# Kernel tuning notes

Measured on AMD Instinct MI355X. Metric: run time of the kernel, lower is better.

The kernel has to match this reference:

```python
import jax, jax.numpy as jnp
import numpy as np

N, E, B = 20000, 100000, 16
U_SZ, U_RED = 4096, 256
EDGE_H, EDGE_OUT = 1024, 512
NODE_H = 512
X_DIM, EA_DIM = 9, 1


def _lin(key, fan_out, fan_in):
    kw, kb = jax.random.split(key)
    s = 1.0 / np.sqrt(fan_in)
    w = jax.random.uniform(kw, (fan_out, fan_in), jnp.float32, -s, s)
    b = jax.random.uniform(kb, (fan_out,), jnp.float32, -s, s)
    return w, b


def setup_inputs() -> dict:
    key = jax.random.key(0)
    ks = jax.random.split(key, 16)
    inp = {}
    inp["x"] = jax.random.normal(ks[0], (N, X_DIM), jnp.float32)
    inp["edge_index"] = jax.random.randint(ks[1], (2, E), 0, N, jnp.int64)
    inp["edge_attr"] = jax.random.normal(ks[2], (E, EA_DIM), jnp.float32)
    inp["u"] = jax.random.normal(ks[3], (B, U_SZ), jnp.float32)
    inp["batch"] = jnp.sort(jax.random.randint(ks[4], (N,), 0, B, jnp.int64))
    # select_dim_reduction: Linear(4096, 256)
    inp["w_sel"], inp["b_sel"] = _lin(ks[5], U_RED, U_SZ)
    # edge MLP: 275 -> 1024 -> 1024 -> 1024 -> 1024 -> 512
    e_in = EA_DIM + 2 * X_DIM + U_RED  # 275
    inp["ew0"], inp["eb0"] = _lin(ks[6], EDGE_H, e_in)
    inp["ew1"], inp["eb1"] = _lin(ks[7], EDGE_H, EDGE_H)
    inp["ew2"], inp["eb2"] = _lin(ks[8], EDGE_H, EDGE_H)
    inp["ew3"], inp["eb3"] = _lin(ks[9], EDGE_H, EDGE_H)
    inp["ew4"], inp["eb4"] = _lin(ks[10], EDGE_OUT, EDGE_H)
    # node_mlp_1: (9+512) -> 512 -> 512 (relu after each)
    inp["nw0"], inp["nb0"] = _lin(ks[11], NODE_H, X_DIM + EDGE_OUT)
    inp["nw1"], inp["nb1"] = _lin(ks[12], NODE_H, NODE_H)
    # node_mlp_2: (9+512+256) -> 512 -> 1
    inp["mw0"], inp["mb0"] = _lin(ks[13], NODE_H, X_DIM + NODE_H + U_RED)
    inp["mw1"], inp["mb1"] = _lin(ks[14], 1, NODE_H)
    return inp


def reference(x, edge_index, edge_attr, u, batch,
              w_sel, b_sel,
              ew0, eb0, ew1, eb1, ew2, eb2, ew3, eb3, ew4, eb4,
              nw0, nb0, nw1, nb1, mw0, mb0, mw1, mb1):
    row, col = edge_index[0], edge_index[1]
    u_r = u @ w_sel.T + b_sel                       # [B, 256]
    eb_idx = batch[row]                             # edge -> graph
    # EdgeModel: cat([src, dest, edge_attr, u[batch]]) -> MLP
    e_in = jnp.concatenate([x[row], x[col], edge_attr, u_r[eb_idx]], axis=1)  # [E,275]
    h = jax.nn.relu(e_in @ ew0.T + eb0)
    h = jax.nn.relu(h @ ew1.T + eb1)
    h = jax.nn.relu(h @ ew2.T + eb2)
    h = jax.nn.relu(h @ ew3.T + eb3)
    edge_out = h @ ew4.T + eb4                      # [E, 512]
    # NodeModel: gather x[col], edge MLP, scatter_mean onto row
    n_in = jnp.concatenate([x[col], edge_out], axis=1)  # [E, 521]
    h = jax.nn.relu(n_in @ nw0.T + nb0)
    h = jax.nn.relu(h @ nw1.T + nb1)                # [E, 512]
    seg_sum = jax.ops.segment_sum(h, row, num_segments=x.shape[0])
    cnt = jax.ops.segment_sum(jnp.ones((h.shape[0],), h.dtype), row, num_segments=x.shape[0])
    agg = seg_sum / jnp.maximum(cnt, 1.0)[:, None]  # scatter_mean
    m_in = jnp.concatenate([x, agg, u_r[batch]], axis=1)  # [N, 777]
    h2 = jax.nn.relu(m_in @ mw0.T + mb0)
    out = h2 @ mw1.T + mb1                          # [N, 1]
    return jnp.squeeze(out)
```

## Files before the change

### kernel.cpp

```cpp
#include <hip/hip_runtime.h>


#define NN 20000
#define EE 100000
#define BB 16

typedef _Float16 f16x8 __attribute__((ext_vector_type(8)));
typedef _Float16 f16x4 __attribute__((ext_vector_type(4)));
typedef float f32x4 __attribute__((ext_vector_type(4)));

__device__ __forceinline__ int clampi(int v, int hi) {
    return v < 0 ? 0 : (v >= hi ? hi - 1 : v);
}

__device__ __forceinline__ void gld_lds16(const void* g, void* l) {
    __builtin_amdgcn_global_load_lds(
        (const __attribute__((address_space(1))) unsigned int*)g,
        (__attribute__((address_space(3))) unsigned int*)l, 16, 0, 0);
}

__global__ __launch_bounds__(256, 2) void gemm256n(
    const _Float16* __restrict__ Ag, const _Float16* __restrict__ Wt,
    int KT, int KTs, const float* __restrict__ bias,
    _Float16* __restrict__ C, int KTo, int ktOff)
{
    __shared__ _Float16 As[16384];
    __shared__ _Float16 Bs[8192];

    const int tid  = threadIdx.x;
    const int lane = tid & 63;
    const int wid  = tid >> 6;
    const int wm   = wid & 1;
    const int wn   = wid >> 1;
    const int l15  = lane & 15;
    const int l4   = (lane >> 4) << 2;

    const int nb  = gridDim.x;
    const int MT2 = gridDim.y;
    int f = blockIdx.y * nb + blockIdx.x;
    const int MT8 = MT2 & ~7;
    int p, c;
    if (f < MT8 * nb) {
        c = (f >> 3) % nb;
        p = (f & 7) + 8 * ((f >> 3) / nb);
    } else {
        int g = f - MT8 * nb;
        p = MT8 + g / nb;
        c = g % nb;
    }

    f32x4 acc[8][4];
#pragma unroll
    for (int i = 0; i < 8; ++i)
#pragma unroll
        for (int j = 0; j < 4; ++j) acc[i][j] = (f32x4){0.f, 0.f, 0.f, 0.f};

    const int kg = (lane >> 4) << 10;

    auto stage = [&](int kt) {
        const int par = (kt & 1);
        const _Float16* a0 = Ag + ((size_t)(2 * p)     * KTs + kt) * 4096 + tid * 8;
        const _Float16* a1 = Ag + ((size_t)(2 * p + 1) * KTs + kt) * 4096 + tid * 8;
        const _Float16* b0 = Wt + ((size_t)c * KT + kt) * 4096 + tid * 8;
        _Float16* dA = As + par * 8192 + wid * 512;
        _Float16* dB = Bs + par * 4096 + wid * 512;
        gld_lds16(a0,        dA);
        gld_lds16(a0 + 2048, dA + 2048);
        gld_lds16(a1,        dA + 4096);
        gld_lds16(a1 + 2048, dA + 6144);
        gld_lds16(b0,        dB);
        gld_lds16(b0 + 2048, dB + 2048);
    };

    stage(0);
    for (int kt = 0; kt < KT; ++kt) {
        if (kt + 1 < KT) {
            stage(kt + 1);
            asm volatile("s_waitcnt vmcnt(6)" ::: "memory");
        } else {
            asm volatile("s_waitcnt vmcnt(0)" ::: "memory");
        }
        __builtin_amdgcn_s_barrier();
        const int par = (kt & 1);
        const _Float16* Ap = As + par * 8192 + wm * 4096 + kg + l15 * 8;
        const _Float16* Bp = Bs + par * 4096 + kg + (wn * 64 + l15) * 8;
        f16x8 af[4], bf[4];
#pragma unroll
        for (int j = 0; j < 4; ++j) bf[j] = *(const f16x8*)(Bp + j * 128);
#pragma unroll
        for (int i = 0; i < 4; ++i) af[i] = *(const f16x8*)(Ap + i * 128);
        __builtin_amdgcn_s_setprio(1);
#pragma unroll
        for (int i = 0; i < 4; ++i)
#pragma unroll
            for (int j = 0; j < 4; ++j)
                acc[i][j] = __builtin_amdgcn_mfma_f32_16x16x32_f16(
                    af[i], bf[j], acc[i][j], 0, 0, 0);
        __builtin_amdgcn_s_setprio(0);
#pragma unroll
        for (int i = 0; i < 4; ++i) af[i] = *(const f16x8*)(Ap + (4 + i) * 128);
        __builtin_amdgcn_s_setprio(1);
#pragma unroll
        for (int i = 0; i < 4; ++i)
#pragma unroll
            for (int j = 0; j < 4; ++j)
                acc[4 + i][j] = __builtin_amdgcn_mfma_f32_16x16x32_f16(
                    af[i], bf[j], acc[4 + i][j], 0, 0, 0);
        __builtin_amdgcn_s_setprio(0);
        __builtin_amdgcn_s_barrier();
    }

    _Float16* tr = As;
#pragma unroll
    for (int pass = 0; pass < 4; ++pass) {
        __syncthreads();
        if (wm == (pass >> 1)) {
            const int fi = (pass & 1) << 2;
#pragma unroll
            for (int i = 0; i < 4; ++i) {
#pragma unroll
                for (int v = 0; v < 4; ++v) {
                    const int lr = i * 16 + l4 + v;
#pragma unroll
                    for (int j = 0; j < 4; ++j) {
                        const int cc = wn * 64 + j * 16 + l15;
                        float val = acc[fi + i][j][v] + bias[c * 128 + cc];
                        val = fmaxf(val, 0.f);
                        tr[lr * 132 + cc] = (_Float16)val;
                    }
                }
            }
        }
        __syncthreads();
#pragma unroll
        for (int it = 0; it < 4; ++it) {
            const int id = it * 256 + tid;
            const int r  = id & 63;
            const int cg = id >> 6;
            f16x4 lo = *(const f16x4*)(tr + r * 132 + cg * 8);
            f16x4 hi = *(const f16x4*)(tr + r * 132 + cg * 8 + 4);
            f16x8 v8;
#pragma unroll
            for (int t = 0; t < 4; ++t) { v8[t] = lo[t]; v8[t + 4] = hi[t]; }
            const int kti = ktOff + c * 4 + (cg >> 2);
            const int mt_out = 2 * p + (pass >> 1);
            const int r128 = ((pass & 1) << 6) + r;
            *(f16x8*)(C + (((size_t)mt_out * KTo + kti) * 4 + (cg & 3)) * 1024
                        + (size_t)r128 * 8) = v8;
        }
    }
}

template <int MODE>
__global__ __launch_bounds__(256, 4) void gemm_blk(
    const _Float16* __restrict__ A,
    const _Float16* __restrict__ Wt,
    int KT, int KTs,
    const float* __restrict__ bias, int ldbias, const int* __restrict__ gbid,
    void* __restrict__ C, int KTo, int ktOff,
    int ldc,
    const int* __restrict__ srow, float* __restrict__ aux,
    int M, int relu)
{
    __shared__ char smem[32768];
    _Float16* As = (_Float16*)smem;
    _Float16* Bs = As + 8192;

    const int tid  = threadIdx.x;
    const int lane = tid & 63;
    const int wid  = tid >> 6;
    const int wm = (wid & 1) << 6;
    const int wn = (wid >> 1) << 6;

    const int nb = gridDim.x;
    const int MT = gridDim.y;
    int f = blockIdx.y * nb + blockIdx.x;
    const int MT8 = MT & ~7;
    int p, c;
    if (f < MT8 * nb) {
        c = (f >> 3) % nb;
        p = (f & 7) + 8 * ((f >> 3) / nb);
    } else {
        int g = f - MT8 * nb;
        p = MT8 + g / nb;
        c = g % nb;
    }

    f32x4 acc[4][4];
#pragma unroll
    for (int i = 0; i < 4; ++i)
#pragma unroll
        for (int j = 0; j < 4; ++j) acc[i][j] = (f32x4){0.f, 0.f, 0.f, 0.f};

    const _Float16* pA = A + (size_t)p * KTs * 4096;
    const _Float16* pB = Wt + (size_t)c * KT * 4096;
    const int cb0 = wid * 64;
    const int cb1 = 256 + wid * 64;
    const int kq  = (lane >> 4) * 128;
    const int l15 = lane & 15;
    const int l4  = (lane >> 4) << 2;

    int kt = 0;
    for (; kt + 2 <= KT; kt += 2) {
        __syncthreads();
        gld_lds16(pA + (size_t)(cb0 + lane) * 8,        As + cb0 * 8);
        gld_lds16(pA + (size_t)(cb1 + lane) * 8,        As + cb1 * 8);
        gld_lds16(pA + 4096 + (size_t)(cb0 + lane) * 8, As + 4096 + cb0 * 8);
        gld_lds16(pA + 4096 + (size_t)(cb1 + lane) * 8, As + 4096 + cb1 * 8);
        gld_lds16(pB + (size_t)(cb0 + lane) * 8,        Bs + cb0 * 8);
        gld_lds16(pB + (size_t)(cb1 + lane) * 8,        Bs + cb1 * 8);
        gld_lds16(pB + 4096 + (size_t)(cb0 + lane) * 8, Bs + 4096 + cb0 * 8);
        gld_lds16(pB + 4096 + (size_t)(cb1 + lane) * 8, Bs + 4096 + cb1 * 8);
        pA += 8192; pB += 8192;
        __syncthreads();

#pragma unroll
        for (int s = 0; s < 2; ++s) {
            f16x8 af[4], bf[4];
            const int sb = s * 4096;
#pragma unroll
            for (int i = 0; i < 4; ++i)
                af[i] = *(const f16x8*)(As + sb + (size_t)((kq + wm + i * 16 + l15) << 3));
#pragma unroll
            for (int j = 0; j < 4; ++j)
                bf[j] = *(const f16x8*)(Bs + sb + (size_t)((kq + wn + j * 16 + l15) << 3));
#pragma unroll
            for (int i = 0; i < 4; ++i)
#pragma unroll
                for (int j = 0; j < 4; ++j)
                    acc[i][j] = __builtin_amdgcn_mfma_f32_16x16x32_f16(af[i], bf[j], acc[i][j], 0, 0, 0);
        }
    }
    if (kt < KT) {
        __syncthreads();
        gld_lds16(pA + (size_t)(cb0 + lane) * 8, As + cb0 * 8);
        gld_lds16(pA + (size_t)(cb1 + lane) * 8, As + cb1 * 8);
        gld_lds16(pB + (size_t)(cb0 + lane) * 8, Bs + cb0 * 8);
        gld_lds16(pB + (size_t)(cb1 + lane) * 8, Bs + cb1 * 8);
        __syncthreads();
        f16x8 af[4], bf[4];
#pragma unroll
        for (int i = 0; i < 4; ++i)
            af[i] = *(const f16x8*)(As + (size_t)((kq + wm + i * 16 + l15) << 3));
#pragma unroll
        for (int j = 0; j < 4; ++j)
            bf[j] = *(const f16x8*)(Bs + (size_t)((kq + wn + j * 16 + l15) << 3));
#pragma unroll
        for (int i = 0; i < 4; ++i)
#pragma unroll
            for (int j = 0; j < 4; ++j)
                acc[i][j] = __builtin_amdgcn_mfma_f32_16x16x32_f16(af[i], bf[j], acc[i][j], 0, 0, 0);
    }

    if (MODE == 0) {
        _Float16* tr = (_Float16*)smem;
#pragma unroll
        for (int pass = 0; pass < 2; ++pass) {
            __syncthreads();
            if (wm == pass * 64) {
#pragma unroll
                for (int i = 0; i < 4; ++i) {
#pragma unroll
                    for (int v = 0; v < 4; ++v) {
                        const int lr = i * 16 + l4 + v;
                        const float* brow = bias;
                        if (gbid) {
                            int m = p * 128 + pass * 64 + lr;
                            if (m >= M) m = M - 1;
                            brow = bias + (size_t)clampi(gbid[m], BB) * ldbias;
                        }
#pragma unroll
                        for (int j = 0; j < 4; ++j) {
                            const int cc = wn + j * 16 + l15;
                            float val = acc[i][j][v] + brow[c * 128 + cc];
                            if (relu) val = fmaxf(val, 0.f);
                            tr[lr * 132 + cc] = (_Float16)val;
                        }
                    }
                }
            }
            __syncthreads();
#pragma unroll
            for (int it = 0; it < 4; ++it) {
                const int id = it * 256 + tid;
                const int r  = id & 63;
                const int cg = id >> 6;
                f16x4 lo = *(const f16x4*)(tr + r * 132 + cg * 8);
                f16x4 hi = *(const f16x4*)(tr + r * 132 + cg * 8 + 4);
                f16x8 v8;
#pragma unroll
                for (int t = 0; t < 4; ++t) { v8[t] = lo[t]; v8[t + 4] = hi[t]; }
                const int kti = ktOff + (c << 2) + (cg >> 2);
                const int gr  = pass * 64 + r;
                size_t o = (((size_t)p * KTo + kti) * 4 + (cg & 3)) * 1024 + (size_t)gr * 8;
                *(f16x8*)((_Float16*)C + o) = v8;
            }
        }
    } else if (MODE == 1) {
#pragma unroll
        for (int i = 0; i < 4; ++i) {
#pragma unroll
            for (int v = 0; v < 4; ++v) {
                const int m = p * 128 + wm + i * 16 + l4 + v;
                if (m >= M) continue;
                const float* brow = bias;
                if (gbid) brow = bias + (size_t)clampi(gbid[m], BB) * ldbias;
#pragma unroll
                for (int j = 0; j < 4; ++j) {
                    const int col = c * 128 + wn + j * 16 + l15;
                    float val = acc[i][j][v] + brow[col];
                    if (relu) val = fmaxf(val, 0.f);
                    ((float*)C)[(size_t)m * ldc + col] = val;
                }
            }
        }
    } else if (MODE == 2) {
        float* trf = (float*)smem;
#pragma unroll
        for (int pass = 0; pass < 4; ++pass) {
            __syncthreads();
            if (wm == ((pass >> 1) << 6)) {
                const int i0 = (pass & 1) << 1;
#pragma unroll
                for (int ii = 0; ii < 2; ++ii) {
                    const int i = i0 + ii;
                    const int lr = ii * 16 + l4;
#pragma unroll
                    for (int v = 0; v < 4; ++v) {
#pragma unroll
                        for (int j = 0; j < 4; ++j) {
                            const int cc = wn + j * 16 + l15;
                            float val = acc[i][j][v] + bias[c * 128 + cc];
                            if (relu) val = fmaxf(val, 0.f);
                            trf[(lr + v) * 130 + cc] = val;
                        }
                    }
                }
            }
            __syncthreads();
            const int ebase = p * 128 + pass * 32;
#pragma unroll
            for (int it = 0; it < 16; ++it) {
                const int id = it * 256 + tid;
                const int lr = id >> 7;
                const int colg = id & 127;
                const int el = ebase + lr;
                if (el < M) {
                    const int node = clampi(srow[el], NN);
                    atomicAdd(&aux[(size_t)node * 512 + c * 128 + colg],
                              trf[lr * 130 + colg]);
                }
            }
        }
    } else {
        const float* mw1 = aux;
        float* out = (float*)C;
#pragma unroll
        for (int i = 0; i < 4; ++i) {
#pragma unroll
            for (int v = 0; v < 4; ++v) {
                const int m = p * 128 + wm + i * 16 + l4 + v;
                const int mc = m < M ? m : M - 1;
                const float* brow = bias + (size_t)clampi(gbid[mc], BB) * ldbias;
                float s = 0.f;
#pragma unroll
                for (int j = 0; j < 4; ++j) {
                    const int col = c * 128 + wn + j * 16 + l15;
                    float val = acc[i][j][v] + brow[col];
                    val = fmaxf(val, 0.f);
                    s += val * mw1[col];
                }
                s += __shfl_down(s, 8, 16);
                s += __shfl_down(s, 4, 16);
                s += __shfl_down(s, 2, 16);
                s += __shfl_down(s, 1, 16);
                if (l15 == 0 && m < M) atomicAdd(&out[m], s);
            }
        }
    }
}


__global__ void k_w2h_blk(const float* __restrict__ src, _Float16* __restrict__ dst,
                          int N, int Ksrc, int Kd, int mode)
{
    int t = blockIdx.x * blockDim.x + threadIdx.x;
    if (t >= N * Kd) return;
    int n = t / Kd, k = t - n * Kd;
    float v = 0.f;
    if (mode == 0)      { if (k < Ksrc) v = src[(size_t)n * Ksrc + k]; }
    else if (mode == 1) { if (k < 19) v = src[(size_t)n * 275 + k]; }
    else if (mode == 2) { if (k < 9) v = src[(size_t)n * Ksrc + k];
                          else if (k >= 32 && k < 544) v = src[(size_t)n * Ksrc + 9 + (k - 32)]; }
    else if (mode == 4) { if (k < Ksrc) v = src[(size_t)k * N + n]; }
    else                { v = src[(size_t)n * Ksrc + 9 + k]; }
    int KT = Kd >> 5;
    int nt = n >> 7, r = n & 127, kt = k >> 5, kg = (k >> 3) & 3, ko = k & 7;
    dst[(((size_t)nt * KT + kt) * 4 + kg) * 1024 + (size_t)r * 8 + ko] = (_Float16)v;
}

__global__ void k_fill_w32(const float* __restrict__ nw0, _Float16* __restrict__ whnc)
{
    int t = blockIdx.x * blockDim.x + threadIdx.x;
    if (t >= 512 * 32) return;
    int n = t >> 5, k = t & 31;
    float v = (k < 9) ? nw0[(size_t)n * 521 + k] : 0.f;
    int nt = n >> 7, r = n & 127, kg = (k >> 3) & 3, ko = k & 7;
    whnc[(((size_t)nt * 33 + 32) * 4 + kg) * 1024 + (size_t)r * 8 + ko] = (_Float16)v;
}

__global__ void k_bfuse(const float* __restrict__ nw0, const float* __restrict__ eb4,
                        const float* __restrict__ nb0, float* __restrict__ bf)
{
    int wave = (blockIdx.x * 256 + threadIdx.x) >> 6;
    int lane = threadIdx.x & 63;
    if (wave >= 512) return;
    const float* wr = nw0 + (size_t)wave * 521 + 9;
    float s = 0.f;
#pragma unroll
    for (int i = 0; i < 8; ++i) s += wr[lane * 8 + i] * eb4[lane * 8 + i];
    for (int off = 32; off; off >>= 1) s += __shfl_down(s, off);
    if (lane == 0) bf[wave] = s + nb0[wave];
}

__global__ void k_u_r(const float* __restrict__ u, const float* __restrict__ w_sel,
                      const float* __restrict__ b_sel, float* __restrict__ u_r)
{
    int wave = (blockIdx.x * 256 + threadIdx.x) >> 6;
    int lane = threadIdx.x & 63;
    int b = wave >> 8, n = wave & 255;
    const float4* u4 = (const float4*)(u + (size_t)b * 4096);
    const float4* w4 = (const float4*)(w_sel + (size_t)n * 4096);
    float s = 0.f;
    for (int i = lane; i < 1024; i += 64) {
        float4 a = u4[i], c = w4[i];
        s += a.x * c.x + a.y * c.y + a.z * c.z + a.w * c.w;
    }
    for (int off = 32; off; off >>= 1) s += __shfl_down(s, off);
    if (lane == 0) u_r[b * 256 + n] = s + b_sel[n];
}

__global__ void k_graph_bias(const float* __restrict__ u_r, const float* __restrict__ w,
                             const float* __restrict__ b, float* __restrict__ ub,
                             int Nout, int Ksrc, int koff)
{
    int wave = (blockIdx.x * 256 + threadIdx.x) >> 6;
    int lane = threadIdx.x & 63;
    if (wave >= 16 * Nout) return;
    int g = wave / Nout, n = wave - g * Nout;
    const float* ur = u_r + (size_t)g * 256;
    const float* wr = w + (size_t)n * Ksrc + koff;
    float s = 0.f;
#pragma unroll
    for (int i = 0; i < 4; ++i) s += ur[lane * 4 + i] * wr[lane * 4 + i];
    for (int off = 32; off; off >>= 1) s += __shfl_down(s, off);
    if (lane == 0) ub[(size_t)g * Nout + n] = s + b[n];
}

__global__ void k_gbe(const int* __restrict__ row, const int* __restrict__ batch,
                      int* __restrict__ gbe, float* __restrict__ cnt)
{
    int e = blockIdx.x * blockDim.x + threadIdx.x;
    if (e >= EE) return;
    int r = clampi(row[e], NN);
    gbe[e] = clampi(batch[r], BB);
    atomicAdd(&cnt[r], 1.f);
}

__global__ void k_init_out(float* __restrict__ out, const float* __restrict__ mb1)
{
    int t = blockIdx.x * blockDim.x + threadIdx.x;
    if (t < NN) out[t] = mb1[0];
}

__global__ void k_gather_edge_blk(const float* __restrict__ x, const float* __restrict__ ea,
                                  const int* __restrict__ row, const int* __restrict__ col,
                                  _Float16* __restrict__ dst, _Float16* __restrict__ pong,
                                  int e0, int ec, int MTR)
{
    int t = blockIdx.x * blockDim.x + threadIdx.x;
    if (t >= MTR * 4) return;
    int r = t >> 2, kg = t & 3;
    int e = e0 + r; int emax = e0 + ec - 1;
    if (e > emax) e = emax;
    int ri = clampi(row[e], NN), ci = clampi(col[e], NN);
    f16x8 v;
    f16x8 vx = (f16x8)(_Float16)0.f;
#pragma unroll
    for (int j = 0; j < 8; ++j) {
        int cc = kg * 8 + j;
        float fv = 0.f;
        if (cc < 9)       fv = x[(size_t)ri * 9 + cc];
        else if (cc < 18) fv = x[(size_t)ci * 9 + (cc - 9)];
        else if (cc == 18) fv = ea[e];
        v[j] = (_Float16)fv;
        if (cc < 9) vx[j] = (_Float16)x[(size_t)ci * 9 + cc];
    }
    *(f16x8*)(dst + (size_t)(r >> 7) * 4096 + (size_t)kg * 1024 + (size_t)(r & 127) * 8) = v;
    *(f16x8*)(pong + (((size_t)(r >> 7) * 33 + 32) * 4 + kg) * 1024 + (size_t)(r & 127) * 8) = vx;
}

__global__ void k_gather_min(const float* __restrict__ x, const float* __restrict__ agg,
                             const float* __restrict__ cnt, _Float16* __restrict__ dst, int MTR)
{
    int t = blockIdx.x * blockDim.x + threadIdx.x;
    if (t >= MTR * 68) return;
    int r = t / 68, q = t - r * 68;
    int kt = q >> 2, kg = q & 3;
    int n = r < NN ? r : NN - 1;
    f16x8 v = (f16x8)(_Float16)0.f;
    if (kt == 0) {
#pragma unroll
        for (int j = 0; j < 8; ++j) {
            int cc = kg * 8 + j;
            if (cc < 9) v[j] = (_Float16)x[(size_t)n * 9 + cc];
        }
    } else {
        float inv = 1.f / fmaxf(cnt[n], 1.f);
        int cbase = (kt - 1) * 32 + kg * 8;
        const float4* ap = (const float4*)(agg + (size_t)n * 512 + cbase);
        float4 a0 = ap[0], a1 = ap[1];
        v[0] = (_Float16)(a0.x * inv); v[1] = (_Float16)(a0.y * inv);
        v[2] = (_Float16)(a0.z * inv); v[3] = (_Float16)(a0.w * inv);
        v[4] = (_Float16)(a1.x * inv); v[5] = (_Float16)(a1.y * inv);
        v[6] = (_Float16)(a1.z * inv); v[7] = (_Float16)(a1.w * inv);
    }
    *(f16x8*)(dst + ((size_t)(r >> 7) * 17 + kt) * 4096 + (size_t)kg * 1024 + (size_t)(r & 127) * 8) = v;
}


#define GRID1(n) dim3(((n) + 255) / 256)

static inline void gemmB0(hipStream_t s, const _Float16* A, const _Float16* Wt, int KT, int KTs,
                          const float* bias, int ldbias, const int* gbid,
                          void* C, int KTo, int ktOff,
                          int M, int MT, int NT, int relu)
{
    hipLaunchKernelGGL(gemm_blk<0>, dim3(NT, MT), dim3(256), 0, s,
                       A, Wt, KT, KTs, bias, ldbias, gbid, C, KTo, ktOff, 0,
                       nullptr, nullptr, M, relu);
}
static inline void gemmB2(hipStream_t s, const _Float16* A, const _Float16* Wt, int KT, int KTs,
                          const float* bias, const int* srow, float* agg,
                          int M, int MT, int NT, int relu)
{
    hipLaunchKernelGGL(gemm_blk<2>, dim3(NT, MT), dim3(256), 0, s,
                       A, Wt, KT, KTs, bias, 0, nullptr, nullptr, 0, 0, 0,
                       srow, agg, M, relu);
}
static inline void gemmB3(hipStream_t s, const _Float16* A, const _Float16* Wt, int KT, int KTs,
                          const float* bias, int ldbias, const int* gbid,
                          float* out, const float* mw1,
                          int M, int MT, int NT)
{
    hipLaunchKernelGGL(gemm_blk<3>, dim3(NT, MT), dim3(256), 0, s,
                       A, Wt, KT, KTs, bias, ldbias, gbid, out, 0, 0, 0,
                       nullptr, (float*)mw1, M, 1);
}

extern "C" void kernel_launch(void* const* d_in, const int* in_sizes, int n_in,
                              void* d_out, int out_size, void* d_ws, size_t ws_size,
                              hipStream_t stream)
{
    const float* x     = (const float*)d_in[0];
    const int*   ei    = (const int*)d_in[1];
    const float* ea    = (const float*)d_in[2];
    const float* u     = (const float*)d_in[3];
    const int*   batch = (const int*)d_in[4];
    const float* w_sel = (const float*)d_in[5];
    const float* b_sel = (const float*)d_in[6];
    const float* ew0 = (const float*)d_in[7];   const float* eb0 = (const float*)d_in[8];
    const float* ew1 = (const float*)d_in[9];   const float* eb1 = (const float*)d_in[10];
    const float* ew2 = (const float*)d_in[11];  const float* eb2 = (const float*)d_in[12];
    const float* ew3 = (const float*)d_in[13];  const float* eb3 = (const float*)d_in[14];
    const float* ew4 = (const float*)d_in[15];  const float* eb4 = (const float*)d_in[16];
    const float* nw0 = (const float*)d_in[17];  const float* nb0 = (const float*)d_in[18];
    const float* nw1 = (const float*)d_in[19];  const float* nb1 = (const float*)d_in[20];
    const float* mw0 = (const float*)d_in[21];  const float* mb0 = (const float*)d_in[22];
    const float* mw1 = (const float*)d_in[23];  const float* mb1 = (const float*)d_in[24];

    const int* row = ei;
    const int* col = ei + EE;

    char* W = (char*)d_ws;
    size_t off = 0;
    auto alloc = [&](size_t bytes) -> char* {
        char* p = W + off;
        off = (off + bytes + 255) & ~(size_t)255;
        return p;
    };
    float*    cnt   = (float*)alloc(20000 * 4);
    float*    agg   = (float*)alloc((size_t)NN * 512 * 4);
    float*    zbias = (float*)alloc(1024 * 4);
    const size_t zeroBytes = off;
    float*    u_r  = (float*)alloc(16 * 256 * 4);
    float*    ub0  = (float*)alloc(16 * 1024 * 4);
    float*    ubm  = (float*)alloc(16 * 512 * 4);
    float*    bfu  = (float*)alloc(512 * 4);
    int*      gbe  = (int*)alloc((size_t)EE * 4);
    _Float16* wh0   = (_Float16*)alloc((size_t)8 * 1 * 4096 * 2);
    _Float16* wh1   = (_Float16*)alloc((size_t)8 * 32 * 4096 * 2);
    _Float16* wh2   = (_Float16*)alloc((size_t)8 * 32 * 4096 * 2);
    _Float16* wh3   = (_Float16*)alloc((size_t)8 * 32 * 4096 * 2);
    _Float16* whnc  = (_Float16*)alloc((size_t)4 * 33 * 4096 * 2);
    _Float16* whn1  = (_Float16*)alloc((size_t)4 * 16 * 4096 * 2);
    _Float16* whm0  = (_Float16*)alloc((size_t)4 * 17 * 4096 * 2);
    _Float16* nw0eoB= (_Float16*)alloc((size_t)4 * 16 * 4096 * 2);
    _Float16* ew4T  = (_Float16*)alloc((size_t)8 * 16 * 4096 * 2);
    const int MTm = (NN + 127) / 128;
    _Float16* m_in = (_Float16*)alloc((size_t)MTm * 17 * 4096 * 2);
    const size_t fixedBytes = off;

    static const int ecOpts[] = {50000, 25000, 12500, 10000, 5000};
    int EC = 5000;
    for (int i = 0; i < 5; ++i) {
        int ec = ecOpts[i];
        size_t MTRc = (size_t)((ec + 255) / 256) * 256;
        size_t need = fixedBytes + MTRc * 64 + 2 * (MTRc * 2112) + 4096;
        if (need <= ws_size) { EC = ec; break; }
    }
    const size_t MTR = (size_t)((EC + 255) / 256) * 256;
    const int MT  = (int)(MTR / 128);
    const int MT2 = (int)(MTR / 256);
    _Float16* e_in = (_Float16*)alloc(MTR * 64);
    _Float16* ping = (_Float16*)alloc(MTR * 2112);
    _Float16* pong = (_Float16*)alloc(MTR * 2112);
    const int NCH = (EE + EC - 1) / EC;

    (void)hipMemsetAsync(W, 0, zeroBytes, stream);
    hipLaunchKernelGGL(k_init_out, GRID1(NN), dim3(256), 0, stream, (float*)d_out, mb1);

    hipLaunchKernelGGL(k_u_r, dim3(1024), dim3(256), 0, stream, u, w_sel, b_sel, u_r);
    hipLaunchKernelGGL(k_graph_bias, GRID1(16 * 1024 * 64), dim3(256), 0, stream,
                       u_r, ew0, eb0, ub0, 1024, 275, 19);
    hipLaunchKernelGGL(k_graph_bias, GRID1(16 * 512 * 64), dim3(256), 0, stream,
                       u_r, mw0, mb0, ubm, 512, 777, 521);
    hipLaunchKernelGGL(k_gbe, GRID1(EE), dim3(256), 0, stream, row, batch, gbe, cnt);
    hipLaunchKernelGGL(k_bfuse, dim3(128), dim3(256), 0, stream, nw0, eb4, nb0, bfu);

    auto pack = [&](const float* w, _Float16* wh, int N, int Ksrc, int Kd, int mode) {
        hipLaunchKernelGGL(k_w2h_blk, GRID1(N * Kd), dim3(256), 0, stream, w, wh, N, Ksrc, Kd, mode);
    };
    pack(ew0, wh0, 1024, 275, 32, 1);
    pack(ew1, wh1, 1024, 1024, 1024, 0);
    pack(ew2, wh2, 1024, 1024, 1024, 0);
    pack(ew3, wh3, 1024, 1024, 1024, 0);
    pack(nw1, whn1, 512, 512, 512, 0);
    pack(mw0, whm0, 512, 777, 544, 2);
    pack(nw0, nw0eoB, 512, 521, 512, 5);
    pack(ew4, ew4T, 1024, 512, 512, 4);
    gemmB0(stream, nw0eoB, ew4T, 16, 16, zbias, 0, nullptr, whnc, 33, 0, 512, 4, 8, 0);
    hipLaunchKernelGGL(k_fill_w32, GRID1(512 * 32), dim3(256), 0, stream, nw0, whnc);

    for (int ch = 0; ch < NCH; ++ch) {
        int e0 = ch * EC;
        int ec = EC; if (e0 + ec > EE) ec = EE - e0;
        hipLaunchKernelGGL(k_gather_edge_blk, GRID1((int)MTR * 4), dim3(256), 0, stream,
                           x, ea, row, col, e_in, pong, e0, ec, (int)MTR);
        gemmB0(stream, e_in, wh0, 1, 1, ub0, 1024, gbe + e0, ping, 33, 0, ec, MT, 8, 1);
        hipLaunchKernelGGL(gemm256n, dim3(8, MT2), dim3(256), 0, stream,
                           ping, wh1, 32, 33, eb1, pong, 33, 0);
        hipLaunchKernelGGL(gemm256n, dim3(8, MT2), dim3(256), 0, stream,
                           pong, wh2, 32, 33, eb2, ping, 33, 0);
        hipLaunchKernelGGL(gemm256n, dim3(8, MT2), dim3(256), 0, stream,
                           ping, wh3, 32, 33, eb3, pong, 33, 0);
        hipLaunchKernelGGL(gemm256n, dim3(4, MT2), dim3(256), 0, stream,
                           pong, whnc, 33, 33, bfu, ping, 16, 0);
        gemmB2(stream, ping, whn1, 16, 16, nb1, row + e0, agg, ec, MT, 4, 1);
    }

    hipLaunchKernelGGL(k_gather_min, GRID1((int)(MTm * 128) * 68), dim3(256), 0, stream,
                       x, agg, cnt, m_in, MTm * 128);
    gemmB3(stream, m_in, whm0, 17, 17, ubm, 512, batch, (float*)d_out, mw1, NN, MTm, 4);
}
```

Before: 1.614 ms.

## Replace 256x128 GEMM with 128x128 tile streaming B fragments from global

The large hidden-layer GEMM kernel now works on 128x128 output tiles instead of 256x128, with a 4-deep LDS ring for A only. B fragments are loaded straight from global memory into double-buffered registers, and the trailing per-iteration barrier is removed. Launch bounds rise to 3 waves per SIMD to improve occupancy and latency hiding. The fused 1024->512 layer moves to the existing gemmB0 path. In exchange, B is reused less across M tiles and global load traffic goes up.

```diff
diff --git a/kernel.cpp b/kernel.cpp
--- a/kernel.cpp
+++ b/kernel.cpp
@@ -19,26 +19,26 @@
         (__attribute__((address_space(3))) unsigned int*)l, 16, 0, 0);
 }
 
-__global__ __launch_bounds__(256, 2) void gemm256n(
+__global__ __launch_bounds__(256, 3) void gemmAD(
     const _Float16* __restrict__ Ag, const _Float16* __restrict__ Wt,
     int KT, int KTs, const float* __restrict__ bias,
     _Float16* __restrict__ C, int KTo, int ktOff)
 {
     __shared__ _Float16 As[16384];
-    __shared__ _Float16 Bs[8192];
 
     const int tid  = threadIdx.x;
     const int lane = tid & 63;
     const int wid  = tid >> 6;
-    const int wm   = wid & 1;
-    const int wn   = wid >> 1;
-    const int l15  = lane & 15;
-    const int l4   = (lane >> 4) << 2;
-
-    const int nb  = gridDim.x;
-    const int MT2 = gridDim.y;
+    const int wm = (wid & 1) << 6;
+    const int wn = (wid >> 1) << 6;
+    const int l15 = lane & 15;
+    const int l4  = (lane >> 4) << 2;
+    const int kg  = (lane >> 4) << 10;
+
+    const int nb = gridDim.x;
+    const int MT = gridDim.y;
     int f = blockIdx.y * nb + blockIdx.x;
-    const int MT8 = MT2 & ~7;
+    const int MT8 = MT & ~7;
     int p, c;
     if (f < MT8 * nb) {
         c = (f >> 3) % nb;
@@ -49,44 +49,44 @@
         c = g % nb;
     }
 
-    f32x4 acc[8][4];
-#pragma unroll
-    for (int i = 0; i < 8; ++i)
+    f32x4 acc[4][4];
+#pragma unroll
+    for (int i = 0; i < 4; ++i)
 #pragma unroll
         for (int j = 0; j < 4; ++j) acc[i][j] = (f32x4){0.f, 0.f, 0.f, 0.f};
 
-    const int kg = (lane >> 4) << 10;
-
-    auto stage = [&](int kt) {
-        const int par = (kt & 1);
-        const _Float16* a0 = Ag + ((size_t)(2 * p)     * KTs + kt) * 4096 + tid * 8;
-        const _Float16* a1 = Ag + ((size_t)(2 * p + 1) * KTs + kt) * 4096 + tid * 8;
-        const _Float16* b0 = Wt + ((size_t)c * KT + kt) * 4096 + tid * 8;
-        _Float16* dA = As + par * 8192 + wid * 512;
-        _Float16* dB = Bs + par * 4096 + wid * 512;
-        gld_lds16(a0,        dA);
-        gld_lds16(a0 + 2048, dA + 2048);
-        gld_lds16(a1,        dA + 4096);
-        gld_lds16(a1 + 2048, dA + 6144);
-        gld_lds16(b0,        dB);
-        gld_lds16(b0 + 2048, dB + 2048);
+    const _Float16* gA = Ag + (size_t)p * KTs * 4096;
+    const _Float16* gB = Wt + ((size_t)c * KT) * 4096 + kg + (wn + l15) * 8;
+    const int ktLim = KT - 1;
+
+    auto stageA = [&](int ktA) {
+        const _Float16* s = gA + (size_t)ktA * 4096 + tid * 8;
+        _Float16* d = As + ((ktA & 3) << 12) + wid * 512;
+        gld_lds16(s, d);
+        gld_lds16(s + 2048, d + 2048);
     };
 
-    stage(0);
-    for (int kt = 0; kt < KT; ++kt) {
-        if (kt + 1 < KT) {
-            stage(kt + 1);
-            asm volatile("s_waitcnt vmcnt(6)" ::: "memory");
-        } else {
-            asm volatile("s_waitcnt vmcnt(0)" ::: "memory");
-        }
+    f16x8 bfA[4], bfB[4];
+    auto loadB = [&](f16x8 (&bf)[4], int ktB) {
+        const _Float16* bp = gB + (size_t)ktB * 4096;
+#pragma unroll
+        for (int j = 0; j < 4; ++j) bf[j] = *(const f16x8*)(bp + j * 128);
+    };
+
+    stageA(0);
+    stageA(1 <= ktLim ? 1 : ktLim);
+    loadB(bfA, 0);
+
+    auto body = [&](int kt, f16x8 (&cur)[4], f16x8 (&nxt)[4]) {
+        const int ktB = kt + 1 <= ktLim ? kt + 1 : ktLim;
+        const int ktA = kt + 2 <= ktLim ? kt + 2 : ktLim;
+        loadB(nxt, ktB);
+        stageA(ktA);
+        asm volatile("s_waitcnt vmcnt(12)" ::: "memory");
         __builtin_amdgcn_s_barrier();
-        const int par = (kt & 1);
-        const _Float16* Ap = As + par * 8192 + wm * 4096 + kg + l15 * 8;
-        const _Float16* Bp = Bs + par * 4096 + kg + (wn * 64 + l15) * 8;
-        f16x8 af[4], bf[4];
-#pragma unroll
-        for (int j = 0; j < 4; ++j) bf[j] = *(const f16x8*)(Bp + j * 128);
+        asm volatile("" ::: "memory");
+        const _Float16* Ap = As + ((kt & 3) << 12) + kg + (wm + l15) * 8;
+        f16x8 af[4];
 #pragma unroll
         for (int i = 0; i < 4; ++i) af[i] = *(const f16x8*)(Ap + i * 128);
         __builtin_amdgcn_s_setprio(1);
@@ -95,27 +95,20 @@
 #pragma unroll
             for (int j = 0; j < 4; ++j)
                 acc[i][j] = __builtin_amdgcn_mfma_f32_16x16x32_f16(
-                    af[i], bf[j], acc[i][j], 0, 0, 0);
+                    af[i], cur[j], acc[i][j], 0, 0, 0);
         __builtin_amdgcn_s_setprio(0);
-#pragma unroll
-        for (int i = 0; i < 4; ++i) af[i] = *(const f16x8*)(Ap + (4 + i) * 128);
-        __builtin_amdgcn_s_setprio(1);
-#pragma unroll
-        for (int i = 0; i < 4; ++i)
-#pragma unroll
-            for (int j = 0; j < 4; ++j)
-                acc[4 + i][j] = __builtin_amdgcn_mfma_f32_16x16x32_f16(
-                    af[i], bf[j], acc[4 + i][j], 0, 0, 0);
-        __builtin_amdgcn_s_setprio(0);
-        __builtin_amdgcn_s_barrier();
+    };
+
+    for (int kt = 0; kt + 2 <= KT; kt += 2) {
+        body(kt,     bfA, bfB);
+        body(kt + 1, bfB, bfA);
     }
 
     _Float16* tr = As;
 #pragma unroll
-    for (int pass = 0; pass < 4; ++pass) {
+    for (int pass = 0; pass < 2; ++pass) {
         __syncthreads();
-        if (wm == (pass >> 1)) {
-            const int fi = (pass & 1) << 2;
+        if (wm == pass * 64) {
 #pragma unroll
             for (int i = 0; i < 4; ++i) {
 #pragma unroll
@@ -123,8 +116,8 @@
                     const int lr = i * 16 + l4 + v;
 #pragma unroll
                     for (int j = 0; j < 4; ++j) {
-                        const int cc = wn * 64 + j * 16 + l15;
-                        float val = acc[fi + i][j][v] + bias[c * 128 + cc];
+                        const int cc = wn + j * 16 + l15;
+                        float val = acc[i][j][v] + bias[c * 128 + cc];
                         val = fmaxf(val, 0.f);
                         tr[lr * 132 + cc] = (_Float16)val;
                     }
@@ -142,11 +135,10 @@
             f16x8 v8;
 #pragma unroll
             for (int t = 0; t < 4; ++t) { v8[t] = lo[t]; v8[t + 4] = hi[t]; }
-            const int kti = ktOff + c * 4 + (cg >> 2);
-            const int mt_out = 2 * p + (pass >> 1);
-            const int r128 = ((pass & 1) << 6) + r;
-            *(f16x8*)(C + (((size_t)mt_out * KTo + kti) * 4 + (cg & 3)) * 1024
-                        + (size_t)r128 * 8) = v8;
+            const int kti = ktOff + (c << 2) + (cg >> 2);
+            const int gr  = pass * 64 + r;
+            size_t o = (((size_t)p * KTo + kti) * 4 + (cg & 3)) * 1024 + (size_t)gr * 8;
+            *(f16x8*)(C + o) = v8;
         }
     }
 }
@@ -621,7 +613,6 @@
     }
     const size_t MTR = (size_t)((EC + 255) / 256) * 256;
     const int MT  = (int)(MTR / 128);
-    const int MT2 = (int)(MTR / 256);
     _Float16* e_in = (_Float16*)alloc(MTR * 64);
     _Float16* ping = (_Float16*)alloc(MTR * 2112);
     _Float16* pong = (_Float16*)alloc(MTR * 2112);
@@ -658,14 +649,13 @@
         hipLaunchKernelGGL(k_gather_edge_blk, GRID1((int)MTR * 4), dim3(256), 0, stream,
                            x, ea, row, col, e_in, pong, e0, ec, (int)MTR);
         gemmB0(stream, e_in, wh0, 1, 1, ub0, 1024, gbe + e0, ping, 33, 0, ec, MT, 8, 1);
-        hipLaunchKernelGGL(gemm256n, dim3(8, MT2), dim3(256), 0, stream,
+        hipLaunchKernelGGL(gemmAD, dim3(8, MT), dim3(256), 0, stream,
                            ping, wh1, 32, 33, eb1, pong, 33, 0);
-        hipLaunchKernelGGL(gemm256n, dim3(8, MT2), dim3(256), 0, stream,
+        hipLaunchKernelGGL(gemmAD, dim3(8, MT), dim3(256), 0, stream,
                            pong, wh2, 32, 33, eb2, ping, 33, 0);
-        hipLaunchKernelGGL(gemm256n, dim3(8, MT2), dim3(256), 0, stream,
+        hipLaunchKernelGGL(gemmAD, dim3(8, MT), dim3(256), 0, stream,
                            ping, wh3, 32, 33, eb3, pong, 33, 0);
-        hipLaunchKernelGGL(gemm256n, dim3(4, MT2), dim3(256), 0, stream,
-                           pong, whnc, 33, 33, bfu, ping, 16, 0);
+        gemmB0(stream, pong, whnc, 33, 33, bfu, 0, nullptr, ping, 16, 0, ec, MT, 4, 1);
         gemmB2(stream, ping, whn1, 16, 16, nb1, row + e0, agg, ec, MT, 4, 1);
     }
 
```

Result: faster. 1.438 ms (-10.9%).
